# Kernel tuning notes

Hardware: AMD Instinct MI355X
Metric: run time of the kernel (lower is better)

## Reference

```python
import jax, jax.numpy as jnp
import numpy as np

B, H, W = 4, 112, 112
N = H * W              # 12544 tokens
NBHD = 48              # local neighborhood size
DIM = 256
OUT_DIM = 512
INNER = 4              # inner_ch of weight_net
TABLE = 4096           # pre_table rows
ALPHA = 4.0
DS_RATE = 0.25
STRIDE = 2
RESERVE = (H // 4) * (W // 4)  # 784 reserve tokens (pos % 4 == 0)
EPS = 1e-5


def _ln(x, g, b):
    m = x.mean(-1, keepdims=True)
    v = ((x - m) ** 2).mean(-1, keepdims=True)
    return (x - m) / jnp.sqrt(v + EPS) * g + b


def setup_inputs() -> dict:
    key = jax.random.key(0)
    ks = jax.random.split(key, 8)
    ii, jj = jnp.meshgrid(jnp.arange(H), jnp.arange(W), indexing='ij')
    pos = jnp.stack([ii, jj], -1).reshape(1, N, 2).astype(jnp.float32)
    pos = jnp.tile(pos, (B, 1, 1))                             # b x n x 2 integer grid
    feat = jax.random.normal(ks[0], (B, N, DIM), jnp.float32)
    member_idx = jax.random.randint(ks[1], (B, N, NBHD), 0, N)
    cluster_mask = (jax.random.uniform(ks[2], (B, N, NBHD)) > 0.1).astype(jnp.float32)
    learned_prob = jax.random.uniform(ks[3], (B, N, 1), dtype=jnp.float32)
    pe_idx = jax.random.randint(ks[4], (B, N, NBHD), 0, TABLE)
    pre_table = jax.random.normal(ks[5], (TABLE, 5), jnp.float32)
    w1 = jax.random.normal(ks[6], (5, INNER), jnp.float32) * 0.4
    b1 = jnp.zeros((INNER,), jnp.float32)
    ln1_g = jnp.ones((INNER,), jnp.float32)
    ln1_b = jnp.zeros((INNER,), jnp.float32)
    norm_g = jnp.ones((INNER * DIM,), jnp.float32)
    norm_b = jnp.zeros((INNER * DIM,), jnp.float32)
    lin_w = jax.random.normal(ks[7], (INNER * DIM, OUT_DIM), jnp.float32) * (1.0 / np.sqrt(INNER * DIM))
    lin_b = jnp.zeros((OUT_DIM,), jnp.float32)
    return dict(pos=pos, feat=feat, member_idx=member_idx, cluster_mask=cluster_mask,
                learned_prob=learned_prob, stride=STRIDE, pe_idx=pe_idx, reserve_num=RESERVE,
                pre_table=pre_table, w1=w1, b1=b1, ln1_g=ln1_g, ln1_b=ln1_b,
                norm_g=norm_g, norm_b=norm_b, lin_w=lin_w, lin_b=lin_b)


def reference(pos, feat, member_idx, cluster_mask, learned_prob, stride, pe_idx,
              reserve_num, pre_table, w1, b1, ln1_g, ln1_b, norm_g, norm_b, lin_w, lin_b):
    b, n, c = feat.shape
    keep_num = int(n * DS_RATE)
    pos_long = pos.astype(jnp.int32)
    # stride == 2 branch: tokens on the coarse grid get prob 1
    grid_prob = jnp.all(pos_long % stride == 0, axis=-1).astype(jnp.float32)      # b x n
    lp_s = jax.lax.stop_gradient(learned_prob).reshape(b, n) * ALPHA              # detached scores
    final_prob = grid_prob + lp_s
    reserve_mask = jnp.all(pos_long % (stride * 2) == 0, axis=-1).astype(jnp.float32)
    final_prob = final_prob + reserve_mask * (-100.0)
    sample_num = keep_num - reserve_num
    _, sample_idx = jax.lax.top_k(final_prob, sample_num)                         # b x sample_num
    # per-row nonzero of reserve_mask (exactly reserve_num hits per row)
    flat_nz = jnp.nonzero(reserve_mask.reshape(-1) > 0, size=b * reserve_num)[0]
    reserve_idx = (flat_nz % n).reshape(b, reserve_num).astype(sample_idx.dtype)
    idx = jnp.concatenate([sample_idx, reserve_idx], axis=1)                      # b x keep_num

    pos_k = jnp.take_along_axis(pos, idx[:, :, None], axis=1)                     # b x keep x 2
    nbhd = member_idx.shape[-1]
    mem_k = jnp.take_along_axis(member_idx, idx[:, :, None], axis=1)              # b x keep x nbhd
    pe_k = jnp.take_along_axis(pe_idx, idx[:, :, None], axis=1)
    cm_k = jnp.take_along_axis(cluster_mask, idx[:, :, None], axis=1)
    lp = jnp.take_along_axis(learned_prob, mem_k.reshape(b, -1, 1), axis=1)
    lp = lp.reshape(b, keep_num, nbhd, 1)

    # weight_net on the small PE table, then gather per-edge weights
    wt = jax.nn.gelu(_ln(pre_table @ w1 + b1, ln1_g, ln1_b), approximate=False)   # TABLE x INNER
    weights = wt[pe_k]                                                            # b x keep x nbhd x INNER
    weights = weights * (lp * cm_k[..., None])

    # CLUSTENWF: gather neighbor features and weighted-sum over the neighborhood
    gathered = jnp.take_along_axis(feat, mem_k.reshape(b, -1, 1), axis=1)
    gathered = gathered.reshape(b, keep_num, nbhd, c)                             # b x keep x nbhd x c
    out = jnp.einsum('bnkm,bnkc->bnmc', weights, gathered).reshape(b, keep_num, INNER * c)
    out = _ln(out, norm_g, norm_b)
    return pos_k, out @ lin_w + lin_b
```

## Files before the change

kernel.cpp:

```cpp
#include <hip/hip_runtime.h>

typedef unsigned short u16;
typedef unsigned int u32;
typedef unsigned long long u64;

#define NB 4
#define NTOK 12544
#define NBHD 48
#define DIM 256
#define OUTD 512
#define KEEPN 3136
#define SAMPLEN 2352
#define RESN 784
#define GW 112
#define POSN (NB * KEEPN * 2)
#define QTR (NTOK / 4)
#define NBKT 16384

#define BLKM 128
#define BLKN 256
#define BROW 40

#define FEATB_BYTES (25690112ull)
#define XWS_BYTES   (25690112ull)
#define LINT_BYTES  (1048576ull)
#define KEYS_BYTES  (401408ull)
#define PART_BYTES  (802816ull)
#define WS_NEED (FEATB_BYTES + XWS_BYTES + LINT_BYTES + KEYS_BYTES + PART_BYTES)

__device__ __forceinline__ float bf2f(u16 u) {
    union { u32 i; float f; } v; v.i = ((u32)u) << 16; return v.f;
}
__device__ __forceinline__ float asf(u32 u) {
    union { u32 i; float f; } v; v.i = u; return v.f;
}
__device__ __forceinline__ u16 f2bf(float f) {
    union { u32 i; float f; } v; v.f = f;
    return (u16)((v.i + 0x7FFFu + ((v.i >> 16) & 1u)) >> 16);
}

typedef __bf16 bf16x8 __attribute__((ext_vector_type(8)));
typedef float floatx4 __attribute__((ext_vector_type(4)));

__device__ __forceinline__ float make_f(float lp, int n) {
    int i = n / GW, j = n % GW;
    float f = lp * 4.0f;
    if (((i | j) & 1) == 0) f = 1.0f + f;
    if (((i | j) & 3) == 0) f = f + (-100.0f);
    return f;
}
__device__ __forceinline__ u64 f_to_key(float f, int n) {
    union { float f; u32 u; } v; v.f = f;
    u32 m = (v.u & 0x80000000u) ? ~v.u : (v.u | 0x80000000u);
    return (((u64)m) << 32) | (u64)(0xFFFFFFFFu - (u32)n);
}
__device__ __forceinline__ int f_to_bucket(float f) {
    int b = (int)floorf(f * 3276.8f);
    return b < 0 ? 0 : (b > NBKT - 1 ? NBKT - 1 : b);
}

__global__ __launch_bounds__(256) void feat_cvt_kernel(
    const float* __restrict__ feat, u16* __restrict__ featb) {
    int t = blockIdx.x * 256 + threadIdx.x;
    float4 v = ((const float4*)feat)[t];
    u64 w = (u64)f2bf(v.x) | ((u64)f2bf(v.y) << 16) |
            ((u64)f2bf(v.z) << 32) | ((u64)f2bf(v.w) << 48);
    ((u64*)featb)[t] = w;
}

__global__ __launch_bounds__(256) void linT_cvt_kernel(
    const float* __restrict__ lin_w, u16* __restrict__ linT,
    u32* __restrict__ hist) {
    __shared__ u16 T[64 * 65];
    int k0 = blockIdx.x * 64, n0 = blockIdx.y * 64;
    int t = threadIdx.x;
    int bid = blockIdx.y * 16 + blockIdx.x;
    hist[bid * 512 + t] = 0;
    hist[bid * 512 + 256 + t] = 0;
    int r = t >> 2, c4 = (t & 3) * 16;
#pragma unroll
    for (int i = 0; i < 4; ++i) {
        float4 v = *(const float4*)&lin_w[(size_t)(k0 + r) * OUTD + n0 + c4 + i * 4];
        T[(c4 + i * 4 + 0) * 65 + r] = f2bf(v.x);
        T[(c4 + i * 4 + 1) * 65 + r] = f2bf(v.y);
        T[(c4 + i * 4 + 2) * 65 + r] = f2bf(v.z);
        T[(c4 + i * 4 + 3) * 65 + r] = f2bf(v.w);
    }
    __syncthreads();
    int nl = t >> 2, kc = (t & 3) * 16;
    union { uint4 v[2]; u16 h[16]; } u;
#pragma unroll
    for (int i = 0; i < 16; ++i) u.h[i] = T[nl * 65 + kc + i];
    u16* dst = &linT[(size_t)(n0 + nl) * 1024 + k0 + kc];
    *(uint4*)(dst + 0) = u.v[0];
    *(uint4*)(dst + 8) = u.v[1];
}

__global__ __launch_bounds__(256) void hist_kernel(
    const float* __restrict__ lprob, u32* __restrict__ hist) {
    int g = blockIdx.x * 256 + threadIdx.x;
    int b = g / NTOK, n = g % NTOK;
    int bkt = f_to_bucket(make_f(lprob[g], n));
    atomicAdd(&hist[b * NBKT + bkt], 1u);
}

__global__ __launch_bounds__(1024) void prefix_kernel(
    const u32* __restrict__ hist, u32* __restrict__ base, u32* __restrict__ cursor) {
    int b = blockIdx.x, t = threadIdx.x;
    const u32* h = hist + b * NBKT;
    u32 loc[16], own = 0;
#pragma unroll
    for (int i = 0; i < 16; ++i) { loc[i] = h[t * 16 + i]; own += loc[i]; }
    __shared__ u32 buf[2][1024];
    buf[0][t] = own;
    __syncthreads();
    int src = 0;
    for (int off = 1; off < 1024; off <<= 1) {
        u32 v = buf[src][t] + ((t + off < 1024) ? buf[src][t + off] : 0u);
        buf[src ^ 1][t] = v;
        src ^= 1;
        __syncthreads();
    }
    u32 above = buf[src][t] - own;
    u32 suf = 0, bout[16];
    for (int i = 15; i >= 0; --i) { bout[i] = above + suf; suf += loc[i]; }
    u32* bb = base + b * NBKT;
    u32* cc = cursor + b * NBKT;
#pragma unroll
    for (int i = 0; i < 16; ++i) { bb[t * 16 + i] = bout[i]; cc[t * 16 + i] = bout[i]; }
}

__global__ __launch_bounds__(256) void scatter_kernel(
    const float* __restrict__ lprob, u32* __restrict__ cursor,
    u64* __restrict__ slots) {
    int g = blockIdx.x * 256 + threadIdx.x;
    int b = g / NTOK, n = g % NTOK;
    float f = make_f(lprob[g], n);
    int bkt = f_to_bucket(f);
    u32 s = atomicAdd(&cursor[b * NBKT + bkt], 1u);
    slots[b * NTOK + s] = f_to_key(f, n);
}

__global__ __launch_bounds__(256) void rank_finalize_kernel(
    const float* __restrict__ lprob, const u32* __restrict__ hist,
    const u32* __restrict__ base, const u64* __restrict__ slots,
    float* __restrict__ pos_out) {
    int g = blockIdx.x * 256 + threadIdx.x;
    int b = g / NTOK, n = g % NTOK;
    int i = n / GW, j = n % GW;
    if (((i | j) & 3) == 0) {
        int r = (i >> 2) * 28 + (j >> 2);
        int slot = b * KEEPN + SAMPLEN + r;
        pos_out[slot * 2 + 0] = (float)i;
        pos_out[slot * 2 + 1] = (float)j;
        return;
    }
    float f = make_f(lprob[g], n);
    int bkt = f_to_bucket(f);
    u32 r0 = base[b * NBKT + bkt];
    if (r0 >= SAMPLEN) return;
    u64 my = f_to_key(f, n);
    u32 cnt = hist[b * NBKT + bkt];
    const u64* sl = slots + b * NTOK + r0;
    u32 rank = r0;
    for (u32 s = 0; s < cnt; ++s) rank += (sl[s] > my) ? 1u : 0u;
    if (rank < SAMPLEN) {
        int slot = b * KEEPN + (int)rank;
        pos_out[slot * 2 + 0] = (float)i;
        pos_out[slot * 2 + 1] = (float)j;
    }
}

#define PSTR 20
__global__ __launch_bounds__(256) void token_v2_kernel(
    const float* __restrict__ pos_in, u16* __restrict__ xdst,
    const int* __restrict__ member_idx, const int* __restrict__ pe_idx,
    const float* __restrict__ cmask, const float* __restrict__ lprob,
    const u16* __restrict__ featb, const float* __restrict__ pre_table,
    const float* __restrict__ w1, const float* __restrict__ b1,
    const float* __restrict__ g1, const float* __restrict__ bb1,
    const float* __restrict__ norm_g, const float* __restrict__ norm_b) {
    int bi = blockIdx.x;
    int xcd = bi & 7, jj = bi >> 3;
    int b = xcd >> 1;
    int t = b * KEEPN + (xcd & 1) * 1568 + jj;
    int tid = threadIdx.x;
    int wave = tid >> 6, lane = tid & 63;
    __shared__ int mem_s[NBHD];
    __shared__ float4 w_s[NBHD];
    __shared__ float partials[4 * 64 * PSTR];
    __shared__ float red[10];

    int n_src = (int)pos_in[t * 2 + 0] * GW + (int)pos_in[t * 2 + 1];

    if (tid < NBHD) {
        int e = (b * NTOK + n_src) * NBHD + tid;
        int mem = member_idx[e];
        int pe = pe_idx[e];
        float cm = cmask[e];
        float lpe = lprob[b * NTOK + mem];
        float z[4];
#pragma unroll
        for (int m = 0; m < 4; ++m) {
            float acc = b1[m];
#pragma unroll
            for (int d = 0; d < 5; ++d) acc += pre_table[pe * 5 + d] * w1[d * 4 + m];
            z[m] = acc;
        }
        float mean = (z[0] + z[1] + z[2] + z[3]) * 0.25f;
        float var = 0.0f;
#pragma unroll
        for (int m = 0; m < 4; ++m) { float d = z[m] - mean; var += d * d; }
        float rstd = rsqrtf(var * 0.25f + 1e-5f);
        float sc = lpe * cm;
        float wv[4];
#pragma unroll
        for (int m = 0; m < 4; ++m) {
            float y = (z[m] - mean) * rstd * g1[m] + bb1[m];
            wv[m] = 0.5f * y * (1.0f + erff(y * 0.70710678118654752f)) * sc;
        }
        w_s[tid] = make_float4(wv[0], wv[1], wv[2], wv[3]);
        mem_s[tid] = mem;
    }
    __syncthreads();

    float acc[16];
#pragma unroll
    for (int i = 0; i < 16; ++i) acc[i] = 0.0f;
    const u16* fbase = featb + (size_t)b * NTOK * DIM + lane * 4;
    int k0 = wave * 12;
#pragma unroll
    for (int kk = 0; kk < 12; ++kk) {
        int k = k0 + kk;
        uint2 d = *(const uint2*)(fbase + (size_t)mem_s[k] * DIM);
        float4 w = w_s[k];
        float c0 = asf(d.x << 16);
        float c1 = asf(d.x & 0xFFFF0000u);
        float c2 = asf(d.y << 16);
        float c3 = asf(d.y & 0xFFFF0000u);
        acc[0]  += w.x * c0; acc[1]  += w.y * c0; acc[2]  += w.z * c0; acc[3]  += w.w * c0;
        acc[4]  += w.x * c1; acc[5]  += w.y * c1; acc[6]  += w.z * c1; acc[7]  += w.w * c1;
        acc[8]  += w.x * c2; acc[9]  += w.y * c2; acc[10] += w.z * c2; acc[11] += w.w * c2;
        acc[12] += w.x * c3; acc[13] += w.y * c3; acc[14] += w.z * c3; acc[15] += w.w * c3;
    }
    float* pp = &partials[(wave * 64 + lane) * PSTR];
#pragma unroll
    for (int i = 0; i < 4; ++i)
        *(float4*)(pp + i * 4) = make_float4(acc[i * 4], acc[i * 4 + 1],
                                             acc[i * 4 + 2], acc[i * 4 + 3]);
    __syncthreads();

    int c = tid;
    float a[4] = {0.f, 0.f, 0.f, 0.f};
#pragma unroll
    for (int w = 0; w < 4; ++w) {
        float4 v = *(const float4*)&partials[(w * 64 + (c >> 2)) * PSTR + (c & 3) * 4];
        a[0] += v.x; a[1] += v.y; a[2] += v.z; a[3] += v.w;
    }

    float s1 = a[0] + a[1] + a[2] + a[3];
    float s2 = a[0] * a[0] + a[1] * a[1] + a[2] * a[2] + a[3] * a[3];
#pragma unroll
    for (int off = 32; off > 0; off >>= 1) {
        s1 += __shfl_down(s1, off, 64);
        s2 += __shfl_down(s2, off, 64);
    }
    if (lane == 0) { red[wave] = s1; red[4 + wave] = s2; }
    __syncthreads();
    if (tid == 0) {
        float S = red[0] + red[1] + red[2] + red[3];
        float Q = red[4] + red[5] + red[6] + red[7];
        float mean = S * (1.0f / 1024.0f);
        float var = fmaxf(Q * (1.0f / 1024.0f) - mean * mean, 0.0f);
        red[8] = mean; red[9] = rsqrtf(var + 1e-5f);
    }
    __syncthreads();
    float mean = red[8], rstd = red[9];
    u16* Xp = xdst + (size_t)t * 1024;
#pragma unroll
    for (int m = 0; m < 4; ++m) {
        int cc = m * 256 + c;
        float v = (a[m] - mean) * rstd * norm_g[cc] + norm_b[cc];
        Xp[cc] = f2bf(v);
    }
}

#define GROW 40
__global__ __launch_bounds__(256) void gemm_tile_kernel(
    const u16* __restrict__ xws, const u16* __restrict__ linT,
    const float* __restrict__ lin_b, float* __restrict__ out) {
    __shared__ __align__(16) u16 As[128 * GROW];
    __shared__ __align__(16) u16 Bs[128 * GROW];
    int tid = threadIdx.x;
    int wave = tid >> 6, lane = tid & 63;
    int l15 = lane & 15, quad = lane >> 4;
    int wm = wave >> 1, wn = wave & 1;
    int m0 = blockIdx.x * 128, n0 = blockIdx.y * 128;
    int sr = tid >> 2, sk = (tid & 3) * 8;

    const u16* Ap0 = xws + (size_t)(m0 + sr) * 1024 + sk;
    const u16* Ap1 = Ap0 + (size_t)64 * 1024;
    const u16* Bp0 = linT + (size_t)(n0 + sr) * 1024 + sk;
    const u16* Bp1 = Bp0 + (size_t)64 * 1024;

    floatx4 acc[4][4] = {};
    for (int kk = 0; kk < 1024; kk += 32) {
        uint4 a0 = *(const uint4*)(Ap0 + kk);
        uint4 a1 = *(const uint4*)(Ap1 + kk);
        uint4 b0 = *(const uint4*)(Bp0 + kk);
        uint4 b1 = *(const uint4*)(Bp1 + kk);
        __syncthreads();
        *(uint4*)&As[sr * GROW + sk] = a0;
        *(uint4*)&As[(64 + sr) * GROW + sk] = a1;
        *(uint4*)&Bs[sr * GROW + sk] = b0;
        *(uint4*)&Bs[(64 + sr) * GROW + sk] = b1;
        __syncthreads();
        bf16x8 af[4], bfv[4];
#pragma unroll
        for (int mi = 0; mi < 4; ++mi)
            af[mi] = *(const bf16x8*)&As[(wm * 64 + mi * 16 + l15) * GROW + quad * 8];
#pragma unroll
        for (int ni = 0; ni < 4; ++ni)
            bfv[ni] = *(const bf16x8*)&Bs[(wn * 64 + ni * 16 + l15) * GROW + quad * 8];
#pragma unroll
        for (int mi = 0; mi < 4; ++mi)
#pragma unroll
            for (int ni = 0; ni < 4; ++ni)
                acc[mi][ni] = __builtin_amdgcn_mfma_f32_16x16x32_bf16(
                    af[mi], bfv[ni], acc[mi][ni], 0, 0, 0);
    }
#pragma unroll
    for (int ni = 0; ni < 4; ++ni) {
        int col = n0 + wn * 64 + ni * 16 + l15;
        float bias = lin_b[col];
#pragma unroll
        for (int mi = 0; mi < 4; ++mi)
#pragma unroll
            for (int reg = 0; reg < 4; ++reg) {
                int row = m0 + wm * 64 + mi * 16 + quad * 4 + reg;
                out[(size_t)row * OUTD + col] = acc[mi][ni][reg] + bias;
            }
    }
}

__global__ __launch_bounds__(256) void key_kernel(
    const float* __restrict__ lprob, u64* __restrict__ keys) {
    int g = blockIdx.x * 256 + threadIdx.x;
    int n = g % NTOK;
    keys[g] = f_to_key(make_f(lprob[g], n), n);
}

__global__ __launch_bounds__(256) void partial_rank_kernel(
    const u64* __restrict__ keys, u32* __restrict__ part) {
    int b = blockIdx.y, z = blockIdx.z;
    int n = blockIdx.x * 256 + threadIdx.x;
    u64 my = keys[b * NTOK + n];
    const u64* kb = keys + b * NTOK + z * QTR;
    u32 cnt = 0;
    for (int t = 0; t < QTR; t += 8) {
#pragma unroll
        for (int j = 0; j < 8; ++j) cnt += (kb[t + j] > my) ? 1u : 0u;
    }
    part[(z * NB + b) * NTOK + n] = cnt;
}

__global__ __launch_bounds__(256) void finalize_kernel(
    const u32* __restrict__ part, float* __restrict__ pos_out) {
    int b = blockIdx.y;
    int n = blockIdx.x * 256 + threadIdx.x;
    int g = b * NTOK + n;
    u32 rank = part[g] + part[(NB + b) * NTOK + n] +
               part[(2 * NB + b) * NTOK + n] + part[(3 * NB + b) * NTOK + n];
    int i = n / GW, j = n % GW;
    if (rank < SAMPLEN) {
        int slot = b * KEEPN + (int)rank;
        pos_out[slot * 2 + 0] = (float)i;
        pos_out[slot * 2 + 1] = (float)j;
    }
    if (((i | j) & 3) == 0) {
        int r = (i >> 2) * 28 + (j >> 2);
        int slot = b * KEEPN + SAMPLEN + r;
        pos_out[slot * 2 + 0] = (float)i;
        pos_out[slot * 2 + 1] = (float)j;
    }
}

__global__ __launch_bounds__(256) void token_fb_kernel(
    const float* __restrict__ pos_in, u16* __restrict__ xdst,
    const int* __restrict__ member_idx, const int* __restrict__ pe_idx,
    const float* __restrict__ cmask, const float* __restrict__ lprob,
    const float* __restrict__ featf, const float* __restrict__ pre_table,
    const float* __restrict__ w1, const float* __restrict__ b1,
    const float* __restrict__ g1, const float* __restrict__ bb1,
    const float* __restrict__ norm_g, const float* __restrict__ norm_b) {
    int t = blockIdx.x;
    int b = t / KEEPN;
    int tid = threadIdx.x;
    __shared__ int mem_s[NBHD];
    __shared__ float4 w_s[NBHD];
    __shared__ float red[10];

    int n_src = (int)pos_in[t * 2 + 0] * GW + (int)pos_in[t * 2 + 1];

    if (tid < NBHD) {
        int e = (b * NTOK + n_src) * NBHD + tid;
        int mem = member_idx[e];
        int pe = pe_idx[e];
        float cm = cmask[e];
        float lpe = lprob[b * NTOK + mem];
        float z[4];
#pragma unroll
        for (int m = 0; m < 4; ++m) {
            float acc = b1[m];
#pragma unroll
            for (int d = 0; d < 5; ++d) acc += pre_table[pe * 5 + d] * w1[d * 4 + m];
            z[m] = acc;
        }
        float mean = (z[0] + z[1] + z[2] + z[3]) * 0.25f;
        float var = 0.0f;
#pragma unroll
        for (int m = 0; m < 4; ++m) { float d = z[m] - mean; var += d * d; }
        float rstd = rsqrtf(var * 0.25f + 1e-5f);
        float sc = lpe * cm;
        float wv[4];
#pragma unroll
        for (int m = 0; m < 4; ++m) {
            float y = (z[m] - mean) * rstd * g1[m] + bb1[m];
            wv[m] = 0.5f * y * (1.0f + erff(y * 0.70710678118654752f)) * sc;
        }
        w_s[tid] = make_float4(wv[0], wv[1], wv[2], wv[3]);
        mem_s[tid] = mem;
    }
    __syncthreads();

    float a0 = 0.f, a1 = 0.f, a2 = 0.f, a3 = 0.f;
    size_t base = (size_t)b * NTOK * DIM + tid;
#pragma unroll 8
    for (int k = 0; k < NBHD; ++k) {
        float g = featf[base + (size_t)mem_s[k] * DIM];
        float4 w = w_s[k];
        a0 += w.x * g; a1 += w.y * g; a2 += w.z * g; a3 += w.w * g;
    }
    float s1 = a0 + a1 + a2 + a3;
    float s2 = a0 * a0 + a1 * a1 + a2 * a2 + a3 * a3;
#pragma unroll
    for (int off = 32; off > 0; off >>= 1) {
        s1 += __shfl_down(s1, off, 64);
        s2 += __shfl_down(s2, off, 64);
    }
    int wave = tid >> 6, lane = tid & 63;
    if (lane == 0) { red[wave] = s1; red[4 + wave] = s2; }
    __syncthreads();
    if (tid == 0) {
        float S = red[0] + red[1] + red[2] + red[3];
        float Q = red[4] + red[5] + red[6] + red[7];
        float mean = S * (1.0f / 1024.0f);
        float var = fmaxf(Q * (1.0f / 1024.0f) - mean * mean, 0.0f);
        red[8] = mean; red[9] = rsqrtf(var + 1e-5f);
    }
    __syncthreads();
    float mean = red[8], rstd = red[9];
    float acc4[4] = {a0, a1, a2, a3};
    u16* Xp = xdst + (size_t)t * 1024;
#pragma unroll
    for (int m = 0; m < 4; ++m) {
        int cc = m * 256 + tid;
        float v = (acc4[m] - mean) * rstd * norm_g[cc] + norm_b[cc];
        Xp[cc] = f2bf(v);
    }
}

__global__ __launch_bounds__(256) void gemm_inplace_kernel(
    const float* __restrict__ lin_w, const float* __restrict__ lin_b,
    float* __restrict__ out) {
    __shared__ __align__(16) u16 Bs[BLKN * BROW];
    int tile_m = blockIdx.x;
    int nblk = blockIdx.y;
    int tid = threadIdx.x;
    int wave = tid >> 6, lane = tid & 63;
    int l15 = lane & 15, quad = lane >> 4;

    const u16* Xbase = (const u16*)out;
    floatx4 acc[8][4] = {};

    for (int kk = 0; kk < 1024; kk += 32) {
        __syncthreads();
#pragma unroll
        for (int it = 0; it < 4; ++it) {
            int task = it * 256 + tid;
            int kp = task >> 6;
            int ng = task & 63;
            int k = kp * 2;
            int n0 = nblk * BLKN + ng * 4;
            float4 fa = *(const float4*)&lin_w[(size_t)(kk + k) * OUTD + n0];
            float4 fb = *(const float4*)&lin_w[(size_t)(kk + k + 1) * OUTD + n0];
            u16* bp = &Bs[(ng * 4) * BROW + k];
            *(u32*)(bp + 0 * BROW) = (u32)f2bf(fa.x) | ((u32)f2bf(fb.x) << 16);
            *(u32*)(bp + 1 * BROW) = (u32)f2bf(fa.y) | ((u32)f2bf(fb.y) << 16);
            *(u32*)(bp + 2 * BROW) = (u32)f2bf(fa.z) | ((u32)f2bf(fb.z) << 16);
            *(u32*)(bp + 3 * BROW) = (u32)f2bf(fa.w) | ((u32)f2bf(fb.w) << 16);
        }
        __syncthreads();
        bf16x8 bfrag[4];
#pragma unroll
        for (int ni = 0; ni < 4; ++ni)
            bfrag[ni] = *(const bf16x8*)&Bs[(wave * 64 + ni * 16 + l15) * BROW + quad * 8];
#pragma unroll
        for (int mi = 0; mi < 8; ++mi) {
            int row = tile_m * BLKM + mi * 16 + l15;
            bf16x8 af = *(const bf16x8*)&Xbase[(size_t)row * 1024 + kk + quad * 8];
#pragma unroll
            for (int ni = 0; ni < 4; ++ni)
                acc[mi][ni] = __builtin_amdgcn_mfma_f32_16x16x32_bf16(
                    af, bfrag[ni], acc[mi][ni], 0, 0, 0);
        }
    }
    __syncthreads();
#pragma unroll
    for (int mi = 0; mi < 8; ++mi)
#pragma unroll
        for (int ni = 0; ni < 4; ++ni) {
            int col = nblk * BLKN + wave * 64 + ni * 16 + l15;
            float bias = lin_b[col];
#pragma unroll
            for (int reg = 0; reg < 4; ++reg) {
                int row = tile_m * BLKM + mi * 16 + quad * 4 + reg;
                out[(size_t)row * OUTD + col] = acc[mi][ni][reg] + bias;
            }
        }
}

extern "C" void kernel_launch(void* const* d_in, const int* in_sizes, int n_in,
                              void* d_out, int out_size, void* d_ws, size_t ws_size,
                              hipStream_t stream) {
    const float* feat     = (const float*)d_in[1];
    const int* member_idx = (const int*)d_in[2];
    const float* cmask    = (const float*)d_in[3];
    const float* lprob    = (const float*)d_in[4];
    const int* pe_idx     = (const int*)d_in[6];
    const float* pre_table= (const float*)d_in[8];
    const float* w1       = (const float*)d_in[9];
    const float* b1       = (const float*)d_in[10];
    const float* g1       = (const float*)d_in[11];
    const float* bb1      = (const float*)d_in[12];
    const float* norm_g   = (const float*)d_in[13];
    const float* norm_b   = (const float*)d_in[14];
    const float* lin_w    = (const float*)d_in[15];
    const float* lin_b    = (const float*)d_in[16];

    float* pos_out = (float*)d_out;
    float* out     = pos_out + POSN;

    if (ws_size >= WS_NEED) {
        char* ws = (char*)d_ws;
        u16* featb = (u16*)ws;
        u16* xws   = (u16*)(ws + FEATB_BYTES);
        u16* linT  = (u16*)(ws + FEATB_BYTES + XWS_BYTES);
        u64* slots = (u64*)(ws + FEATB_BYTES + XWS_BYTES + LINT_BYTES);
        u32* hist  = (u32*)(ws + FEATB_BYTES + XWS_BYTES + LINT_BYTES + KEYS_BYTES);
        u32* base  = hist + NB * NBKT;
        u32* curs  = base + NB * NBKT;

        feat_cvt_kernel<<<12544, 256, 0, stream>>>(feat, featb);
        linT_cvt_kernel<<<dim3(16, 8), 256, 0, stream>>>(lin_w, linT, hist);
        hist_kernel<<<(NB * NTOK) / 256, 256, 0, stream>>>(lprob, hist);
        prefix_kernel<<<NB, 1024, 0, stream>>>(hist, base, curs);
        scatter_kernel<<<(NB * NTOK) / 256, 256, 0, stream>>>(lprob, curs, slots);
        rank_finalize_kernel<<<(NB * NTOK) / 256, 256, 0, stream>>>(
            lprob, hist, base, slots, pos_out);
        token_v2_kernel<<<NB * KEEPN, 256, 0, stream>>>(
            pos_out, xws, member_idx, pe_idx, cmask, lprob, featb,
            pre_table, w1, b1, g1, bb1, norm_g, norm_b);
        gemm_tile_kernel<<<dim3(98, 4), 256, 0, stream>>>(xws, linT, lin_b, out);
    } else {
        u64* keys = (u64*)out;
        u32* part = (u32*)((char*)out + 401408);

        key_kernel<<<(NB * NTOK) / 256, 256, 0, stream>>>(lprob, keys);
        partial_rank_kernel<<<dim3(49, NB, 4), 256, 0, stream>>>(keys, part);
        finalize_kernel<<<dim3(49, NB), 256, 0, stream>>>(part, pos_out);
        token_fb_kernel<<<NB * KEEPN, 256, 0, stream>>>(
            pos_out, (u16*)out, member_idx, pe_idx, cmask, lprob, feat,
            pre_table, w1, b1, g1, bb1, norm_g, norm_b);
        gemm_inplace_kernel<<<dim3(98, 2), 256, 0, stream>>>(lin_w, lin_b, out);
    }
}
```

Measured before the change: 253.2 us.

## Precompute PE weight table once, map one token per wave, remap GEMM tiles per XCD

Computes the weight_net table (linear, layernorm, GELU) once per table row inside the lin_w transpose kernel and stores it in the output buffer. The token kernel then just looks up four weights per edge instead of recomputing them for every edge. It also now gives each token to a single wave that loops over all 48 neighbours, so the cross-wave shared-memory reduction and most block barriers go away, and it writes packed 64-bit outputs. The GEMM launch becomes 1D, with tiles grouped so each XCD handles consecutive row tiles for L2 locality. The cost is that each wave now does four times the serial gather loop, and the output buffer is used as scratch before the GEMM overwrites it.

```diff
diff --git a/kernel.cpp b/kernel.cpp
--- a/kernel.cpp
+++ b/kernel.cpp
@@ -13,6 +13,7 @@
 #define SAMPLEN 2352
 #define RESN 784
 #define GW 112
+#define TABLE 4096
 #define POSN (NB * KEEPN * 2)
 #define QTR (NTOK / 4)
 #define NBKT 16384
@@ -70,13 +71,39 @@
 
 __global__ __launch_bounds__(256) void linT_cvt_kernel(
     const float* __restrict__ lin_w, u16* __restrict__ linT,
-    u32* __restrict__ hist) {
+    u32* __restrict__ hist,
+    const float* __restrict__ pre_table, const float* __restrict__ w1,
+    const float* __restrict__ b1, const float* __restrict__ g1,
+    const float* __restrict__ bb1, float* __restrict__ wt) {
     __shared__ u16 T[64 * 65];
     int k0 = blockIdx.x * 64, n0 = blockIdx.y * 64;
     int t = threadIdx.x;
     int bid = blockIdx.y * 16 + blockIdx.x;
     hist[bid * 512 + t] = 0;
     hist[bid * 512 + 256 + t] = 0;
+    int gid = bid * 256 + t;
+    if (gid < TABLE) {
+        float z[4];
+#pragma unroll
+        for (int m = 0; m < 4; ++m) {
+            float acc = b1[m];
+#pragma unroll
+            for (int d = 0; d < 5; ++d) acc += pre_table[gid * 5 + d] * w1[d * 4 + m];
+            z[m] = acc;
+        }
+        float mean = (z[0] + z[1] + z[2] + z[3]) * 0.25f;
+        float var = 0.0f;
+#pragma unroll
+        for (int m = 0; m < 4; ++m) { float d = z[m] - mean; var += d * d; }
+        float rstd = rsqrtf(var * 0.25f + 1e-5f);
+        float wv[4];
+#pragma unroll
+        for (int m = 0; m < 4; ++m) {
+            float y = (z[m] - mean) * rstd * g1[m] + bb1[m];
+            wv[m] = 0.5f * y * (1.0f + erff(y * 0.70710678118654752f));
+        }
+        *(float4*)&wt[gid * 4] = make_float4(wv[0], wv[1], wv[2], wv[3]);
+    }
     int r = t >> 2, c4 = (t & 3) * 16;
 #pragma unroll
     for (int i = 0; i < 4; ++i) {
@@ -171,56 +198,35 @@
     }
 }
 
-#define PSTR 20
-__global__ __launch_bounds__(256) void token_v2_kernel(
+__global__ __launch_bounds__(256) void token_v3_kernel(
     const float* __restrict__ pos_in, u16* __restrict__ xdst,
     const int* __restrict__ member_idx, const int* __restrict__ pe_idx,
     const float* __restrict__ cmask, const float* __restrict__ lprob,
-    const u16* __restrict__ featb, const float* __restrict__ pre_table,
-    const float* __restrict__ w1, const float* __restrict__ b1,
-    const float* __restrict__ g1, const float* __restrict__ bb1,
+    const u16* __restrict__ featb, const float* __restrict__ wt,
     const float* __restrict__ norm_g, const float* __restrict__ norm_b) {
     int bi = blockIdx.x;
     int xcd = bi & 7, jj = bi >> 3;
     int b = xcd >> 1;
-    int t = b * KEEPN + (xcd & 1) * 1568 + jj;
     int tid = threadIdx.x;
     int wave = tid >> 6, lane = tid & 63;
-    __shared__ int mem_s[NBHD];
-    __shared__ float4 w_s[NBHD];
-    __shared__ float partials[4 * 64 * PSTR];
-    __shared__ float red[10];
-
-    int n_src = (int)pos_in[t * 2 + 0] * GW + (int)pos_in[t * 2 + 1];
-
-    if (tid < NBHD) {
-        int e = (b * NTOK + n_src) * NBHD + tid;
+    int t = b * KEEPN + (xcd & 1) * 1568 + jj * 4 + wave;
+
+    __shared__ float4 w_s[4][NBHD];
+    __shared__ int mem_s[4][NBHD];
+
+    float2 pp = *(const float2*)&pos_in[t * 2];
+    int n_src = (int)pp.x * GW + (int)pp.y;
+
+    if (lane < NBHD) {
+        int e = (b * NTOK + n_src) * NBHD + lane;
         int mem = member_idx[e];
         int pe = pe_idx[e];
         float cm = cmask[e];
         float lpe = lprob[b * NTOK + mem];
-        float z[4];
-#pragma unroll
-        for (int m = 0; m < 4; ++m) {
-            float acc = b1[m];
-#pragma unroll
-            for (int d = 0; d < 5; ++d) acc += pre_table[pe * 5 + d] * w1[d * 4 + m];
-            z[m] = acc;
-        }
-        float mean = (z[0] + z[1] + z[2] + z[3]) * 0.25f;
-        float var = 0.0f;
-#pragma unroll
-        for (int m = 0; m < 4; ++m) { float d = z[m] - mean; var += d * d; }
-        float rstd = rsqrtf(var * 0.25f + 1e-5f);
+        float4 w4 = *(const float4*)&wt[pe * 4];
         float sc = lpe * cm;
-        float wv[4];
-#pragma unroll
-        for (int m = 0; m < 4; ++m) {
-            float y = (z[m] - mean) * rstd * g1[m] + bb1[m];
-            wv[m] = 0.5f * y * (1.0f + erff(y * 0.70710678118654752f)) * sc;
-        }
-        w_s[tid] = make_float4(wv[0], wv[1], wv[2], wv[3]);
-        mem_s[tid] = mem;
+        w_s[wave][lane] = make_float4(w4.x * sc, w4.y * sc, w4.z * sc, w4.w * sc);
+        mem_s[wave][lane] = mem;
     }
     __syncthreads();
 
@@ -228,12 +234,10 @@
 #pragma unroll
     for (int i = 0; i < 16; ++i) acc[i] = 0.0f;
     const u16* fbase = featb + (size_t)b * NTOK * DIM + lane * 4;
-    int k0 = wave * 12;
-#pragma unroll
-    for (int kk = 0; kk < 12; ++kk) {
-        int k = k0 + kk;
-        uint2 d = *(const uint2*)(fbase + (size_t)mem_s[k] * DIM);
-        float4 w = w_s[k];
+#pragma unroll 6
+    for (int k = 0; k < NBHD; ++k) {
+        uint2 d = *(const uint2*)(fbase + (size_t)mem_s[wave][k] * DIM);
+        float4 w = w_s[wave][k];
         float c0 = asf(d.x << 16);
         float c1 = asf(d.x & 0xFFFF0000u);
         float c2 = asf(d.y << 16);
@@ -243,45 +247,31 @@
         acc[8]  += w.x * c2; acc[9]  += w.y * c2; acc[10] += w.z * c2; acc[11] += w.w * c2;
         acc[12] += w.x * c3; acc[13] += w.y * c3; acc[14] += w.z * c3; acc[15] += w.w * c3;
     }
-    float* pp = &partials[(wave * 64 + lane) * PSTR];
-#pragma unroll
-    for (int i = 0; i < 4; ++i)
-        *(float4*)(pp + i * 4) = make_float4(acc[i * 4], acc[i * 4 + 1],
-                                             acc[i * 4 + 2], acc[i * 4 + 3]);
-    __syncthreads();
-
-    int c = tid;
-    float a[4] = {0.f, 0.f, 0.f, 0.f};
-#pragma unroll
-    for (int w = 0; w < 4; ++w) {
-        float4 v = *(const float4*)&partials[(w * 64 + (c >> 2)) * PSTR + (c & 3) * 4];
-        a[0] += v.x; a[1] += v.y; a[2] += v.z; a[3] += v.w;
-    }
-
-    float s1 = a[0] + a[1] + a[2] + a[3];
-    float s2 = a[0] * a[0] + a[1] * a[1] + a[2] * a[2] + a[3] * a[3];
+
+    float s1 = 0.0f, s2 = 0.0f;
+#pragma unroll
+    for (int i = 0; i < 16; ++i) { s1 += acc[i]; s2 += acc[i] * acc[i]; }
 #pragma unroll
     for (int off = 32; off > 0; off >>= 1) {
-        s1 += __shfl_down(s1, off, 64);
-        s2 += __shfl_down(s2, off, 64);
-    }
-    if (lane == 0) { red[wave] = s1; red[4 + wave] = s2; }
-    __syncthreads();
-    if (tid == 0) {
-        float S = red[0] + red[1] + red[2] + red[3];
-        float Q = red[4] + red[5] + red[6] + red[7];
-        float mean = S * (1.0f / 1024.0f);
-        float var = fmaxf(Q * (1.0f / 1024.0f) - mean * mean, 0.0f);
-        red[8] = mean; red[9] = rsqrtf(var + 1e-5f);
-    }
-    __syncthreads();
-    float mean = red[8], rstd = red[9];
+        s1 += __shfl_xor(s1, off, 64);
+        s2 += __shfl_xor(s2, off, 64);
+    }
+    float mean = s1 * (1.0f / 1024.0f);
+    float var = fmaxf(s2 * (1.0f / 1024.0f) - mean * mean, 0.0f);
+    float rstd = rsqrtf(var + 1e-5f);
+
     u16* Xp = xdst + (size_t)t * 1024;
 #pragma unroll
     for (int m = 0; m < 4; ++m) {
-        int cc = m * 256 + c;
-        float v = (a[m] - mean) * rstd * norm_g[cc] + norm_b[cc];
-        Xp[cc] = f2bf(v);
+        int cc = m * 256 + lane * 4;
+        float4 g4 = *(const float4*)&norm_g[cc];
+        float4 b4 = *(const float4*)&norm_b[cc];
+        u16 h0 = f2bf((acc[0 * 4 + m] - mean) * rstd * g4.x + b4.x);
+        u16 h1 = f2bf((acc[1 * 4 + m] - mean) * rstd * g4.y + b4.y);
+        u16 h2 = f2bf((acc[2 * 4 + m] - mean) * rstd * g4.z + b4.z);
+        u16 h3 = f2bf((acc[3 * 4 + m] - mean) * rstd * g4.w + b4.w);
+        u64 w = (u64)h0 | ((u64)h1 << 16) | ((u64)h2 << 32) | ((u64)h3 << 48);
+        *(u64*)(Xp + cc) = w;
     }
 }
 
@@ -291,11 +281,15 @@
     const float* __restrict__ lin_b, float* __restrict__ out) {
     __shared__ __align__(16) u16 As[128 * GROW];
     __shared__ __align__(16) u16 Bs[128 * GROW];
+    int bid = blockIdx.x;
+    int xcd = bid & 7, kk8 = bid >> 3;
+    int tile = xcd * 49 + kk8;
+    int m0 = (tile >> 2) * 128, n0 = (tile & 3) * 128;
+
     int tid = threadIdx.x;
     int wave = tid >> 6, lane = tid & 63;
     int l15 = lane & 15, quad = lane >> 4;
     int wm = wave >> 1, wn = wave & 1;
-    int m0 = blockIdx.x * 128, n0 = blockIdx.y * 128;
     int sr = tid >> 2, sk = (tid & 3) * 8;
 
     const u16* Ap0 = xws + (size_t)(m0 + sr) * 1024 + sk;
@@ -560,18 +554,20 @@
         u32* hist  = (u32*)(ws + FEATB_BYTES + XWS_BYTES + LINT_BYTES + KEYS_BYTES);
         u32* base  = hist + NB * NBKT;
         u32* curs  = base + NB * NBKT;
+        float* wtbuf = out;
 
         feat_cvt_kernel<<<12544, 256, 0, stream>>>(feat, featb);
-        linT_cvt_kernel<<<dim3(16, 8), 256, 0, stream>>>(lin_w, linT, hist);
+        linT_cvt_kernel<<<dim3(16, 8), 256, 0, stream>>>(
+            lin_w, linT, hist, pre_table, w1, b1, g1, bb1, wtbuf);
         hist_kernel<<<(NB * NTOK) / 256, 256, 0, stream>>>(lprob, hist);
         prefix_kernel<<<NB, 1024, 0, stream>>>(hist, base, curs);
         scatter_kernel<<<(NB * NTOK) / 256, 256, 0, stream>>>(lprob, curs, slots);
         rank_finalize_kernel<<<(NB * NTOK) / 256, 256, 0, stream>>>(
             lprob, hist, base, slots, pos_out);
-        token_v2_kernel<<<NB * KEEPN, 256, 0, stream>>>(
+        token_v3_kernel<<<(NB * KEEPN) / 4, 256, 0, stream>>>(
             pos_out, xws, member_idx, pe_idx, cmask, lprob, featb,
-            pre_table, w1, b1, g1, bb1, norm_g, norm_b);
-        gemm_tile_kernel<<<dim3(98, 4), 256, 0, stream>>>(xws, linT, lin_b, out);
+            wtbuf, norm_g, norm_b);
+        gemm_tile_kernel<<<392, 256, 0, stream>>>(xws, linT, lin_b, out);
     } else {
         u64* keys = (u64*)out;
         u32* part = (u32*)((char*)out + 401408);
```

Result: faster. 247.6 us (-2.2%).
